# Performance work log

Hardware: AMD Instinct MI355X
Metric: run time of the kernel (lower is better)

## Reference

```python
import jax, jax.numpy as jnp
import numpy as np

NEG_SLOPE = 0.01  # torch nn.LeakyReLU default


def setup_inputs() -> dict:
    key = jax.random.key(0)
    k1, k2 = jax.random.split(key)
    B, L, N = 32, 512, 1024
    X = jax.random.normal(k1, (B, L, N), dtype=jnp.float32)
    W = jax.random.normal(k2, (1, 2 * L), dtype=jnp.float32) * (1.0 / np.sqrt(2 * L))
    return {"X": X, "W": W}


def reference(X, W):
    # X: [B, L, N]; W: [1, 2L] weight of Linear(2L, 1, bias=False)
    L = X.shape[1]
    N = X.shape[2]
    w1 = W[0, :L]   # applied to X[:, :, i]
    w2 = W[0, L:]   # applied to X[:, :, j]
    s1 = jnp.einsum('bln,l->bn', X, w1)  # [B, N]
    s2 = jnp.einsum('bln,l->bn', X, w2)  # [B, N]
    # e[b,i,j] = leaky_relu(s1[b,i] + s2[b,j]) for i != j, 0 on the diagonal
    e = jax.nn.leaky_relu(s1[:, :, None] + s2[:, None, :], NEG_SLOPE)  # [B, N, N]
    diag = jnp.eye(N, dtype=bool)
    e = jnp.where(diag[None, :, :], 0.0, e)
    # softmax over dim=1 (over i), matching torch.softmax(e, dim=1)
    alpha = jax.nn.softmax(e, axis=1)  # [B, N, N]
    # h = bmm(alpha, X^T)^T: h[b,l,i] = sum_j alpha[b,i,j] * X[b,l,j]
    h = jnp.einsum('bij,blj->bli', alpha, X)  # [B, L, N]
    return jax.nn.sigmoid(h)
```

## Files before the change

### kernel.cpp

```cpp
#include <hip/hip_runtime.h>
#include <hip/hip_bf16.h>

#define BATCH 32
#define LSEQ  512
#define NDIM  1024
#define NSPLIT 16

typedef __attribute__((ext_vector_type(8))) short bf16x8;
typedef __attribute__((ext_vector_type(4))) float f32x4;

__device__ __forceinline__ unsigned short f2bf(float x) {
    __hip_bfloat16 h = __float2bfloat16(x);
    return __builtin_bit_cast(unsigned short, h);
}

__global__ __launch_bounds__(256) void prep_kernel(
    const float* __restrict__ X, const float* __restrict__ W,
    unsigned short* __restrict__ Xb, float* __restrict__ P1, float* __restrict__ P2)
{
    __shared__ float sw[2 * LSEQ];
    int tid = threadIdx.x;
    for (int i = tid; i < 2 * LSEQ; i += 256) sw[i] = W[i];
    __syncthreads();

    int b  = blockIdx.y;
    int sp = blockIdx.x;
    int l0 = sp * (LSEQ / NSPLIT);
    size_t base = ((size_t)b * LSEQ + l0) * NDIM + tid * 4;
    const float* xp = X + base;
    unsigned short* xbp = Xb + base;

    float a0=0,a1=0,a2=0,a3=0, c0=0,c1=0,c2=0,c3=0;
    for (int l = 0; l < LSEQ / NSPLIT; ++l) {
        float4 x = *(const float4*)(xp + (size_t)l * NDIM);
        float w1 = sw[l0 + l], w2 = sw[LSEQ + l0 + l];
        a0 = fmaf(x.x, w1, a0); a1 = fmaf(x.y, w1, a1);
        a2 = fmaf(x.z, w1, a2); a3 = fmaf(x.w, w1, a3);
        c0 = fmaf(x.x, w2, c0); c1 = fmaf(x.y, w2, c1);
        c2 = fmaf(x.z, w2, c2); c3 = fmaf(x.w, w2, c3);
        ushort4 u; u.x = f2bf(x.x); u.y = f2bf(x.y); u.z = f2bf(x.z); u.w = f2bf(x.w);
        *(ushort4*)(xbp + (size_t)l * NDIM) = u;
    }
    size_t po = ((size_t)sp * BATCH + b) * NDIM + tid * 4;
    *(float4*)(P1 + po) = make_float4(a0, a1, a2, a3);
    *(float4*)(P2 + po) = make_float4(c0, c1, c2, c3);
}

__global__ __launch_bounds__(256) void stats_kernel(
    const float* __restrict__ P1, const float* __restrict__ P2,
    float* __restrict__ s1, float* __restrict__ s2, float* __restrict__ lrd)
{
    __shared__ float s1s[NDIM];
    __shared__ float s2s[128];
    int t = threadIdx.x;
    int b = blockIdx.x >> 3, sl = blockIdx.x & 7;
    int j0 = sl * 128;

    #pragma unroll
    for (int q = 0; q < 4; ++q) {
        int n = q * 256 + t;
        float a = 0.f;
        #pragma unroll
        for (int sp = 0; sp < NSPLIT; ++sp)
            a += P1[((size_t)sp * BATCH + b) * NDIM + n];
        s1s[n] = a;
        if (sl == 0) s1[b * NDIM + n] = a;
    }
    if (t < 128) {
        int j = j0 + t;
        float c = 0.f;
        #pragma unroll
        for (int sp = 0; sp < NSPLIT; ++sp)
            c += P2[((size_t)sp * BATCH + b) * NDIM + j];
        s2s[t] = c;
        s2[b * NDIM + j] = c;
    }
    __syncthreads();

    int jl = t >> 1, half = t & 1;
    int jg = j0 + jl;
    float s2j = s2s[jl];
    float sum = 0.f;
    int i0 = half * 512;
    for (int i = i0; i < i0 + 512; ++i) {
        float v = s1s[i] + s2j;
        v = fmaxf(v, 0.01f * v);
        if (i == jg) v = 0.f;
        sum += __expf(v);
    }
    sum += __shfl_xor(sum, 1);
    if (half == 0) lrd[b * NDIM + jg] = -__logf(sum);
}

#define WAITVM0() asm volatile("s_waitcnt vmcnt(0)" ::: "memory")
#define LGKM0()   asm volatile("s_waitcnt lgkmcnt(0)" ::: "memory")
#define BARF()    do { asm volatile("" ::: "memory");                          \
                       __builtin_amdgcn_s_barrier();                           \
                       asm volatile("" ::: "memory"); } while (0)

#define STAGE(DN) {                                                            \
    _Pragma("unroll")                                                          \
    for (int j = 0; j < 4; ++j) {                                              \
        __builtin_amdgcn_global_load_lds(                                      \
            (const __attribute__((address_space(1))) void*)srcp[j],            \
            (__attribute__((address_space(3))) void*)(LdsC + (DN) * 16384 +    \
                tid * 16 + j * 4096), 16, 0, 0);                               \
        srcp[j] += 64;                               \
    } }

#define BGEN(TT, DN) {                                                         \
    int k0f = (TT) * 32;                                                       \
    const float* s2p = s2s + k0f + jb8;                                        \
    const float* ldp = lrds + k0f + jb8;                                       \
    float4 sa = *(const float4*)(s2p);                                         \
    float4 sb = *(const float4*)(s2p + 4);                                     \
    float4 la = *(const float4*)(ldp);                                         \
    float4 lb = *(const float4*)(ldp + 4);                                     \
    float sv[8] = {sa.x,sa.y,sa.z,sa.w,sb.x,sb.y,sb.z,sb.w};                   \
    float lv[8] = {la.x,la.y,la.z,la.w,lb.x,lb.y,lb.z,lb.w};                   \
    _Pragma("unroll")                                                          \
    for (int q2 = 0; q2 < 2; ++q2) {                                           \
        int ig = n0 + rloc0 + q2 * 64;                                         \
        float s1i = s1v[q2];                                                   \
        bf16x8 w;                                                              \
        _Pragma("unroll")                                                      \
        for (int h = 0; h < 8; ++h) {                                          \
            float v = s1i + sv[h];                                             \
            v = fmaxf(v, 0.01f * v);                           \
            if (k0f + jb8 + h == ig) v = 0.f;            \
            w[h] = (short)f2bf(__expf(v + lv[h]));                             \
        }                                                                      \
        *(bf16x8*)(LdsC + 32768 + (DN) * 8192 + srbase + q2 * 4096 + bgin) = w;\
    } }

#define COMPUTE(DD) {                                                          \
    const char* La = LdsC + (DD) * 16384;                                      \
    const char* Lb = LdsC + 32768 + (DD) * 8192;                               \
    bf16x8 av[8], bv[4];                                                       \
    _Pragma("unroll")                                                          \
    for (int mi = 0; mi < 8; ++mi)                                             \
        av[mi] = *(const bf16x8*)(La + abase0 + mi * 1024);                    \
    _Pragma("unroll")                                                          \
    for (int ni = 0; ni < 4; ++ni)                                             \
        bv[ni] = *(const bf16x8*)(Lb + bbase0 + ni * 1024);                    \
    __builtin_amdgcn_s_setprio(1);                                             \
    _Pragma("unroll")                                                          \
    for (int ni = 0; ni < 4; ++ni)                                             \
        _Pragma("unroll")                                                      \
        for (int mi = 0; mi < 8; ++mi)                                         \
            acc[mi][ni] = __builtin_amdgcn_mfma_f32_16x16x32_bf16(             \
                av[mi], bv[ni], acc[mi][ni], 0, 0, 0);                         \
    __builtin_amdgcn_s_setprio(0);                                             \
}

__global__ __launch_bounds__(256, 2) void gemm_kernel(
    const unsigned short* __restrict__ Xb, const float* __restrict__ s1,
    const float* __restrict__ s2, const float* __restrict__ lrd,
    float* __restrict__ out)
{
    __shared__ __align__(16) char LdsC[57344];
    float* s2s  = (float*)(LdsC + 49152);
    float* lrds = (float*)(LdsC + 53248);

    const int tid = threadIdx.x, lane = tid & 63, wid = tid >> 6;
    const int wm = wid >> 1, wn = wid & 1;

    int flat  = blockIdx.x;
    int xcd   = flat & 7;
    int p     = flat >> 3;
    int b     = (p >> 4) * 8 + xcd;
    int inner = p & 15;
    int mt = inner & 1, nt = inner >> 1;
    int l0 = mt * 256, n0 = nt * 128;

    const char* XgB = (const char*)(Xb + ((size_t)b * LSEQ + l0) * NDIM);

    const char* srcp[4];
    #pragma unroll
    for (int j = 0; j < 4; ++j) {
        int c = tid + j * 256;
        int sr = c >> 3, slot = c & 7;
        int li = (slot * 16) ^ ((sr & 7) << 4);
        int r = sr * 2 + (li >> 6);
        srcp[j] = XgB + (size_t)r * 2048 + (li & 63);
    }

    const int rsel = lane & 15, kq = lane >> 4;
    const int finner = (((rsel & 1) * 64) + kq * 16) ^ (((rsel >> 1) & 7) << 4);
    const int abase0 = (wm * 64 + (rsel >> 1)) * 128 + finner;
    const int bbase0 = (wn * 32 + (rsel >> 1)) * 128 + finner;

    const int rloc0 = wid * 16 + (lane & 15);
    const int jb8   = (lane >> 4) * 8;
    const int srbase = (rloc0 >> 1) * 128;
    const int bgin  = (((rloc0 & 1) * 64) + (lane >> 4) * 16)
                      ^ (((rloc0 >> 1) & 7) << 4);

    {
        const float* s2g = s2 + (size_t)b * NDIM;
        const float* ldg = lrd + (size_t)b * NDIM;
        *(float4*)(s2s + tid * 4)  = *(const float4*)(s2g + tid * 4);
        *(float4*)(lrds + tid * 4) = *(const float4*)(ldg + tid * 4);
    }
    STAGE(0);
    __syncthreads();

    float s1v[2];
    s1v[0] = s1[(size_t)b * NDIM + n0 + rloc0];
    s1v[1] = s1[(size_t)b * NDIM + n0 + rloc0 + 64];

    f32x4 acc[8][4] = {};

    BGEN(0, 0);
    LGKM0(); BARF();

    for (int t = 0; t < 31; ++t) {
        int d = t & 1, dn = d ^ 1;
        STAGE(dn);
        BGEN(t + 1, dn);
        COMPUTE(d);
        LGKM0(); WAITVM0(); BARF();
    }
    COMPUTE(1);

    float* outb = out + ((size_t)b * LSEQ + l0) * NDIM + n0;
    const int rq = lane >> 4, cl = lane & 15;
    #pragma unroll
    for (int mi = 0; mi < 8; ++mi)
        #pragma unroll
        for (int ni = 0; ni < 4; ++ni) {
            int col = wn * 64 + ni * 16 + cl;
            #pragma unroll
            for (int r2 = 0; r2 < 4; ++r2) {
                int row = wm * 128 + mi * 16 + rq * 4 + r2;
                float v = acc[mi][ni][r2];
                outb[(size_t)row * NDIM + col] = 1.0f / (1.0f + __expf(-v));
            }
        }
}

#undef WAITVM0
#undef LGKM0
#undef BARF
#undef STAGE
#undef BGEN
#undef COMPUTE

extern "C" void kernel_launch(void* const* d_in, const int* in_sizes, int n_in,
                              void* d_out, int out_size, void* d_ws, size_t ws_size,
                              hipStream_t stream) {
    (void)in_sizes; (void)n_in; (void)out_size; (void)ws_size;
    const float* X = (const float*)d_in[0];
    const float* W = (const float*)d_in[1];
    float* out = (float*)d_out;

    float* s1 = (float*)d_ws;
    float* s2 = s1 + BATCH * NDIM;
    float* lrd = s2 + BATCH * NDIM;
    float* P1 = lrd + BATCH * NDIM;
    float* P2 = P1 + (size_t)NSPLIT * BATCH * NDIM;
    unsigned short* Xb = (unsigned short*)(P2 + (size_t)NSPLIT * BATCH * NDIM);

    prep_kernel<<<dim3(NSPLIT, BATCH), 256, 0, stream>>>(X, W, Xb, P1, P2);
    stats_kernel<<<256, 256, 0, stream>>>(P1, P2, s1, s2, lrd);
    gemm_kernel<<<512, 256, 0, stream>>>(Xb, s1, s2, lrd, out);
}
```

Measured before the change: 173.5 us.

## Widen GEMM blocks to 512 threads covering full L, triple-buffer A tiles, use exp2

The GEMM kernel now uses 512-thread blocks that each cover all 512 L rows for one 128-column tile. The softmax weight tile is generated once per block and shared by 8 waves instead of being built separately in two blocks. The A stream is triple-buffered with a partial vmcnt wait so loads run two stages ahead. The exponent path is rescaled into base 2 (s1, s2 and the log-denominator are pre-scaled by log2e) so the raw v_exp_f32 instruction can be used. The cost is much higher LDS use (120KB), which likely limits occupancy to one block per CU, and the grid halves to 256 blocks.

```diff
diff --git a/kernel.cpp b/kernel.cpp
--- a/kernel.cpp
+++ b/kernel.cpp
@@ -5,6 +5,7 @@
 #define LSEQ  512
 #define NDIM  1024
 #define NSPLIT 16
+#define LOG2E 1.4426950408889634f
 
 typedef __attribute__((ext_vector_type(8))) short bf16x8;
 typedef __attribute__((ext_vector_type(4))) float f32x4;
@@ -12,6 +13,12 @@
 __device__ __forceinline__ unsigned short f2bf(float x) {
     __hip_bfloat16 h = __float2bfloat16(x);
     return __builtin_bit_cast(unsigned short, h);
+}
+
+__device__ __forceinline__ float exp2_fast(float x) {
+    float r;
+    asm("v_exp_f32 %0, %1" : "=v"(r) : "v"(x));
+    return r;
 }
 
 __global__ __launch_bounds__(256) void prep_kernel(
@@ -64,7 +71,7 @@
         for (int sp = 0; sp < NSPLIT; ++sp)
             a += P1[((size_t)sp * BATCH + b) * NDIM + n];
         s1s[n] = a;
-        if (sl == 0) s1[b * NDIM + n] = a;
+        if (sl == 0) s1[b * NDIM + n] = a * LOG2E;
     }
     if (t < 128) {
         int j = j0 + t;
@@ -73,7 +80,7 @@
         for (int sp = 0; sp < NSPLIT; ++sp)
             c += P2[((size_t)sp * BATCH + b) * NDIM + j];
         s2s[t] = c;
-        s2[b * NDIM + j] = c;
+        s2[b * NDIM + j] = c * LOG2E;
     }
     __syncthreads();
 
@@ -89,53 +96,49 @@
         sum += __expf(v);
     }
     sum += __shfl_xor(sum, 1);
-    if (half == 0) lrd[b * NDIM + jg] = -__logf(sum);
-}
-
-#define WAITVM0() asm volatile("s_waitcnt vmcnt(0)" ::: "memory")
+    if (half == 0) lrd[b * NDIM + jg] = -__log2f(sum);
+}
+
+#define WAITVM(n) asm volatile("s_waitcnt vmcnt(" #n ")" ::: "memory")
 #define LGKM0()   asm volatile("s_waitcnt lgkmcnt(0)" ::: "memory")
 #define BARF()    do { asm volatile("" ::: "memory");                          \
                        __builtin_amdgcn_s_barrier();                           \
                        asm volatile("" ::: "memory"); } while (0)
 
-#define STAGE(DN) {                                                            \
+#define STAGE(AB) {                                                            \
     _Pragma("unroll")                                                          \
     for (int j = 0; j < 4; ++j) {                                              \
         __builtin_amdgcn_global_load_lds(                                      \
             (const __attribute__((address_space(1))) void*)srcp[j],            \
-            (__attribute__((address_space(3))) void*)(LdsC + (DN) * 16384 +    \
-                tid * 16 + j * 4096), 16, 0, 0);                               \
+            (__attribute__((address_space(3))) void*)(LdsC + (AB) * 32768 +    \
+                tid * 16 + j * 8192), 16, 0, 0);                               \
         srcp[j] += 64;                               \
     } }
 
 #define BGEN(TT, DN) {                                                         \
     int k0f = (TT) * 32;                                                       \
-    const float* s2p = s2s + k0f + jb8;                                        \
-    const float* ldp = lrds + k0f + jb8;                                       \
+    const float* s2p = s2s + k0f + kc8;                                        \
+    const float* ldp = lrds + k0f + kc8;                                       \
     float4 sa = *(const float4*)(s2p);                                         \
     float4 sb = *(const float4*)(s2p + 4);                                     \
     float4 la = *(const float4*)(ldp);                                         \
     float4 lb = *(const float4*)(ldp + 4);                                     \
     float sv[8] = {sa.x,sa.y,sa.z,sa.w,sb.x,sb.y,sb.z,sb.w};                   \
     float lv[8] = {la.x,la.y,la.z,la.w,lb.x,lb.y,lb.z,lb.w};                   \
-    _Pragma("unroll")                                                          \
-    for (int q2 = 0; q2 < 2; ++q2) {                                           \
-        int ig = n0 + rloc0 + q2 * 64;                                         \
-        float s1i = s1v[q2];                                                   \
-        bf16x8 w;                                                              \
-        _Pragma("unroll")                                                      \
-        for (int h = 0; h < 8; ++h) {                                          \
-            float v = s1i + sv[h];                                             \
-            v = fmaxf(v, 0.01f * v);                           \
-            if (k0f + jb8 + h == ig) v = 0.f;            \
-            w[h] = (short)f2bf(__expf(v + lv[h]));                             \
-        }                                                                      \
-        *(bf16x8*)(LdsC + 32768 + (DN) * 8192 + srbase + q2 * 4096 + bgin) = w;\
-    } }
-
-#define COMPUTE(DD) {                                                          \
-    const char* La = LdsC + (DD) * 16384;                                      \
-    const char* Lb = LdsC + 32768 + (DD) * 8192;                               \
+    bf16x8 w;                                                                  \
+    _Pragma("unroll")                                                          \
+    for (int h = 0; h < 8; ++h) {                                              \
+        float v = s1i + sv[h];                                                 \
+        v = fmaxf(v, 0.01f * v);                   \
+        if (k0f + kc8 + h == ig) v = 0.f;                \
+        w[h] = (short)f2bf(exp2_fast(v + lv[h]));                              \
+    }                                                                          \
+    *(bf16x8*)(LdsC + 98304 + (DN) * 8192 + bgoff) = w;                        \
+}
+
+#define COMPUTE(AB, BD) {                                                      \
+    const char* La = LdsC + (AB) * 32768;                                      \
+    const char* Lb = LdsC + 98304 + (BD) * 8192;                               \
     bf16x8 av[8], bv[4];                                                       \
     _Pragma("unroll")                                                          \
     for (int mi = 0; mi < 8; ++mi)                                             \
@@ -153,14 +156,14 @@
     __builtin_amdgcn_s_setprio(0);                                             \
 }
 
-__global__ __launch_bounds__(256, 2) void gemm_kernel(
+__global__ __launch_bounds__(512, 2) void gemm_kernel(
     const unsigned short* __restrict__ Xb, const float* __restrict__ s1,
     const float* __restrict__ s2, const float* __restrict__ lrd,
     float* __restrict__ out)
 {
-    __shared__ __align__(16) char LdsC[57344];
-    float* s2s  = (float*)(LdsC + 49152);
-    float* lrds = (float*)(LdsC + 53248);
+    __shared__ __align__(16) char LdsC[122880];
+    float* s2s  = (float*)(LdsC + 114688);
+    float* lrds = (float*)(LdsC + 118784);
 
     const int tid = threadIdx.x, lane = tid & 63, wid = tid >> 6;
     const int wm = wid >> 1, wn = wid & 1;
@@ -168,17 +171,16 @@
     int flat  = blockIdx.x;
     int xcd   = flat & 7;
     int p     = flat >> 3;
-    int b     = (p >> 4) * 8 + xcd;
-    int inner = p & 15;
-    int mt = inner & 1, nt = inner >> 1;
-    int l0 = mt * 256, n0 = nt * 128;
-
-    const char* XgB = (const char*)(Xb + ((size_t)b * LSEQ + l0) * NDIM);
+    int b     = (p >> 3) * 8 + xcd;
+    int nt    = p & 7;
+    int n0    = nt * 128;
+
+    const char* XgB = (const char*)(Xb + (size_t)b * LSEQ * NDIM);
 
     const char* srcp[4];
     #pragma unroll
     for (int j = 0; j < 4; ++j) {
-        int c = tid + j * 256;
+        int c = tid + j * 512;
         int sr = c >> 3, slot = c & 7;
         int li = (slot * 16) ^ ((sr & 7) << 4);
         int r = sr * 2 + (li >> 6);
@@ -190,40 +192,40 @@
     const int abase0 = (wm * 64 + (rsel >> 1)) * 128 + finner;
     const int bbase0 = (wn * 32 + (rsel >> 1)) * 128 + finner;
 
-    const int rloc0 = wid * 16 + (lane & 15);
-    const int jb8   = (lane >> 4) * 8;
-    const int srbase = (rloc0 >> 1) * 128;
-    const int bgin  = (((rloc0 & 1) * 64) + (lane >> 4) * 16)
-                      ^ (((rloc0 >> 1) & 7) << 4);
+    const int rr   = wid * 16 + (lane & 15);
+    const int kc8  = (lane >> 4) * 8;
+    const int ig   = n0 + rr;
+    const int bgoff = (rr >> 1) * 128 +
+                      ((((rr & 1) * 64) + (lane >> 4) * 16) ^ (((rr >> 1) & 7) << 4));
 
     {
         const float* s2g = s2 + (size_t)b * NDIM;
         const float* ldg = lrd + (size_t)b * NDIM;
-        *(float4*)(s2s + tid * 4)  = *(const float4*)(s2g + tid * 4);
-        *(float4*)(lrds + tid * 4) = *(const float4*)(ldg + tid * 4);
-    }
-    STAGE(0);
+        if (tid < 256) *(float4*)(s2s + tid * 4) = *(const float4*)(s2g + tid * 4);
+        else *(float4*)(lrds + (tid - 256) * 4) = *(const float4*)(ldg + (tid - 256) * 4);
+    }
+    float s1i = s1[(size_t)b * NDIM + ig];
+
+    STAGE(0); STAGE(1);
     __syncthreads();
-
-    float s1v[2];
-    s1v[0] = s1[(size_t)b * NDIM + n0 + rloc0];
-    s1v[1] = s1[(size_t)b * NDIM + n0 + rloc0 + 64];
 
     f32x4 acc[8][4] = {};
 
     BGEN(0, 0);
     LGKM0(); BARF();
 
-    for (int t = 0; t < 31; ++t) {
-        int d = t & 1, dn = d ^ 1;
-        STAGE(dn);
-        BGEN(t + 1, dn);
-        COMPUTE(d);
-        LGKM0(); WAITVM0(); BARF();
-    }
-    COMPUTE(1);
-
-    float* outb = out + ((size_t)b * LSEQ + l0) * NDIM + n0;
+    for (int t = 0; t < 30; ++t) {
+        STAGE((t + 2) % 3);
+        BGEN(t + 1, (t + 1) & 1);
+        COMPUTE(t % 3, t & 1);
+        WAITVM(4); LGKM0(); BARF();
+    }
+    BGEN(31, 1);
+    COMPUTE(0, 0);
+    WAITVM(0); LGKM0(); BARF();
+    COMPUTE(1, 1);
+
+    float* outb = out + (size_t)b * LSEQ * NDIM + n0;
     const int rq = lane >> 4, cl = lane & 15;
     #pragma unroll
     for (int mi = 0; mi < 8; ++mi)
@@ -239,7 +241,7 @@
         }
 }
 
-#undef WAITVM0
+#undef WAITVM
 #undef LGKM0
 #undef BARF
 #undef STAGE
@@ -263,5 +265,5 @@
 
     prep_kernel<<<dim3(NSPLIT, BATCH), 256, 0, stream>>>(X, W, Xb, P1, P2);
     stats_kernel<<<256, 256, 0, stream>>>(P1, P2, s1, s2, lrd);
-    gemm_kernel<<<512, 256, 0, stream>>>(Xb, s1, s2, lrd, out);
-}
+    gemm_kernel<<<256, 512, 0, stream>>>(Xb, s1, s2, lrd, out);
+}
```

Measured after the change: 176.6 us. No clear change (+1.8%).
